# Kernel tuning notes

Measured on AMD Instinct MI355X. Metric: run time of the kernel, lower is better.

The kernel has to match this reference:

```python
import jax, jax.numpy as jnp
import numpy as np

B, N, E, C = 8, 4096, 1024, 512


def setup_inputs() -> dict:
    key = jax.random.key(0)
    k1, k2, k3, k4 = jax.random.split(key, 4)
    node_feats = jax.random.normal(k1, (B, N, C), dtype=jnp.float32)
    hyper_feats = jax.random.normal(k2, (B, E, C), dtype=jnp.float32)
    # torch nn.Linear params: weight [out, in], bias [out]
    Wq = jax.random.normal(k3, (C, C), dtype=jnp.float32) * (1.0 / np.sqrt(C))
    bq = jnp.zeros((C,), dtype=jnp.float32)
    Wkv = jax.random.normal(k4, (2 * C, C), dtype=jnp.float32) * (1.0 / np.sqrt(C))
    bkv = jnp.zeros((2 * C,), dtype=jnp.float32)
    return {"node_feats": node_feats, "hyper_feats": hyper_feats,
            "Wq": Wq, "bq": bq, "Wkv": Wkv, "bkv": bkv}


def reference(node_feats, hyper_feats, Wq, bq, Wkv, bkv):
    C_ = node_feats.shape[-1]
    scale = C_ ** -0.5
    Q = node_feats @ Wq.T + bq                      # [B,N,C]
    KV = hyper_feats @ Wkv.T + bkv                  # [B,E,2C]
    K, V = KV[..., :C_], KV[..., C_:]               # [B,E,C] each
    attn = jnp.einsum('bnc,bec->bne', Q, K) * scale  # [B,N,E]
    attn = jax.nn.softmax(attn, axis=-1)
    return jnp.einsum('bne,bec->bnc', attn, V)       # [B,N,C]
```

## Files before the change

### kernel.cpp

```cpp
#include <hip/hip_runtime.h>
#include <cstdint>
#include <cstddef>

typedef _Float16 h16;
typedef _Float16 h16x8 __attribute__((ext_vector_type(8)));
typedef float fx4 __attribute__((ext_vector_type(4)));

static constexpr int B_ = 8, N_ = 4096, E_ = 1024, C_ = 512;
static constexpr float SCALE = 0.044194173824159216f;

__device__ __forceinline__ void glds16(const h16* g, h16* l) {
  __builtin_amdgcn_global_load_lds(
      (const __attribute__((address_space(1))) unsigned int*)g,
      (__attribute__((address_space(3))) unsigned int*)l, 16, 0, 0);
}

__global__ __launch_bounds__(256) void cvt_kernel(const float* __restrict__ src,
                                                  h16* __restrict__ dst, int n8) {
  int i = blockIdx.x * 256 + threadIdx.x;
  if (i >= n8) return;
  const float4* s4 = (const float4*)src;
  float4 a = s4[2 * i], b = s4[2 * i + 1];
  h16x8 o;
  o[0] = (h16)a.x; o[1] = (h16)a.y; o[2] = (h16)a.z; o[3] = (h16)a.w;
  o[4] = (h16)b.x; o[5] = (h16)b.y; o[6] = (h16)b.z; o[7] = (h16)b.w;
  *(h16x8*)(dst + (size_t)i * 8) = o;
}

template <int MODE>
__global__ __launch_bounds__(256) void gemm_bt(
    const h16* __restrict__ A, const h16* __restrict__ Bm,
    const float* __restrict__ bias,
    h16* __restrict__ outH, h16* __restrict__ outK, h16* __restrict__ outV,
    float* __restrict__ outF,
    int Ncols, int K) {
  __shared__ h16 sA[128 * 32];
  __shared__ h16 sB[128 * 32];
  const int tid = threadIdx.x;
  const int wave = tid >> 6, lane = tid & 63;
  const int wm = wave >> 1, wn = wave & 1;
  const int lr = lane & 15, kq = lane >> 4;
  const int mBase = blockIdx.x * 128, nBase = blockIdx.y * 128;
  const int z = blockIdx.z;
  if (MODE == 2) { A += (size_t)z * N_ * C_; Bm += (size_t)z * E_ * C_; outH += (size_t)z * N_ * E_; }
  if (MODE == 3) { A += (size_t)z * N_ * E_; Bm += (size_t)z * C_ * E_; outF += (size_t)z * N_ * C_; }

  fx4 acc[4][4];
#pragma unroll
  for (int i = 0; i < 4; i++)
#pragma unroll
    for (int j = 0; j < 4; j++) acc[i][j] = (fx4){0.f, 0.f, 0.f, 0.f};

  const int rowInA = lane >> 2, colInA = (lane & 3) * 8;

  for (int kb = 0; kb < K; kb += 32) {
    __syncthreads();
#pragma unroll
    for (int i = 0; i < 2; i++) {
      int chunk = wave + i * 4;
      glds16(A + (size_t)(mBase + chunk * 16 + rowInA) * K + kb + colInA,
             &sA[chunk * 512]);
      glds16(Bm + (size_t)(nBase + chunk * 16 + rowInA) * K + kb + colInA,
             &sB[chunk * 512]);
    }
    __syncthreads();
    h16x8 af[4], bf[4];
#pragma unroll
    for (int mi = 0; mi < 4; mi++)
      af[mi] = *(const h16x8*)&sA[(wm * 64 + mi * 16 + lr) * 32 + kq * 8];
#pragma unroll
    for (int ni = 0; ni < 4; ni++)
      bf[ni] = *(const h16x8*)&sB[(wn * 64 + ni * 16 + lr) * 32 + kq * 8];
#pragma unroll
    for (int mi = 0; mi < 4; mi++)
#pragma unroll
      for (int ni = 0; ni < 4; ni++)
        acc[mi][ni] = __builtin_amdgcn_mfma_f32_16x16x32_f16(af[mi], bf[ni], acc[mi][ni], 0, 0, 0);
  }

  const int rb = kq * 4;
#pragma unroll
  for (int mi = 0; mi < 4; mi++) {
#pragma unroll
    for (int ni = 0; ni < 4; ni++) {
#pragma unroll
      for (int r = 0; r < 4; r++) {
        int row = mBase + wm * 64 + mi * 16 + rb + r;
        int col = nBase + wn * 64 + ni * 16 + lr;
        float v = acc[mi][ni][r];
        if (MODE == 0) {
          outH[(size_t)row * Ncols + col] = (h16)(v + bias[col]);
        } else if (MODE == 1) {
          v += bias[col];
          if (col < C_) outK[(size_t)row * C_ + col] = (h16)v;
          else          outV[(size_t)row * C_ + (col - C_)] = (h16)v;
        } else if (MODE == 2) {
          outH[(size_t)row * Ncols + col] = (h16)(v * SCALE);
        } else {
          outF[(size_t)row * Ncols + col] = v;
        }
      }
    }
  }
}

__global__ __launch_bounds__(256) void transpose_v(const h16* __restrict__ V,
                                                   h16* __restrict__ Vt) {
  __shared__ float t[64][65];
  int z = blockIdx.z;
  const h16* Vb = V + (size_t)z * E_ * C_;
  h16* Tb = Vt + (size_t)z * C_ * E_;
  int e0 = blockIdx.x * 64, c0 = blockIdx.y * 64;
  int tr = threadIdx.x >> 6, tc = threadIdx.x & 63;
#pragma unroll
  for (int p = 0; p < 16; p++)
    t[p * 4 + tr][tc] = (float)Vb[(size_t)(e0 + p * 4 + tr) * C_ + c0 + tc];
  __syncthreads();
#pragma unroll
  for (int p = 0; p < 16; p++)
    Tb[(size_t)(c0 + p * 4 + tr) * E_ + e0 + tc] = (h16)t[tc][p * 4 + tr];
}

__global__ __launch_bounds__(256) void softmax_rows(h16* __restrict__ S) {
  int row = blockIdx.x * 4 + (threadIdx.x >> 6);
  int lane = threadIdx.x & 63;
  h16* p = S + (size_t)row * E_ + lane * 16;
  h16x8 q0 = *(const h16x8*)p;
  h16x8 q1 = *(const h16x8*)(p + 8);
  float v[16];
#pragma unroll
  for (int j = 0; j < 8; j++) { v[j] = (float)q0[j]; v[8 + j] = (float)q1[j]; }
  float m = v[0];
#pragma unroll
  for (int j = 1; j < 16; j++) m = fmaxf(m, v[j]);
#pragma unroll
  for (int off = 32; off > 0; off >>= 1) m = fmaxf(m, __shfl_xor(m, off));
  float s = 0.f;
#pragma unroll
  for (int j = 0; j < 16; j++) { v[j] = __expf(v[j] - m); s += v[j]; }
#pragma unroll
  for (int off = 32; off > 0; off >>= 1) s += __shfl_xor(s, off);
  float inv = 1.f / s;
  h16x8 o0, o1;
#pragma unroll
  for (int j = 0; j < 8; j++) { o0[j] = (h16)(v[j] * inv); o1[j] = (h16)(v[8 + j] * inv); }
  *(h16x8*)p = o0;
  *(h16x8*)(p + 8) = o1;
}

extern "C" void kernel_launch(void* const* d_in, const int* in_sizes, int n_in,
                              void* d_out, int out_size, void* d_ws, size_t ws_size,
                              hipStream_t stream) {
  const float* node  = (const float*)d_in[0];
  const float* hyper = (const float*)d_in[1];
  const float* Wq    = (const float*)d_in[2];
  const float* bq    = (const float*)d_in[3];
  const float* Wkv   = (const float*)d_in[4];
  const float* bkv   = (const float*)d_in[5];
  float* out = (float*)d_out;
  char* ws = (char*)d_ws;

  h16* node_h  = (h16*)(ws + 0);
  h16* hyper_h = (h16*)(ws + 33554432);
  h16* Wq_h    = (h16*)(ws + 41943040);
  h16* Wkv_h   = (h16*)(ws + 42467328);
  h16* V_h     = (h16*)(ws + 43515904);
  h16* S_h     = (h16*)(ws + 0);
  h16* Q_h     = (h16*)(ws + 67108864);
  h16* K_h     = (h16*)(ws + 100663296);
  h16* Vt_h    = (h16*)(ws + 109051904);
  if (ws_size < 117440512u) return;

  cvt_kernel<<<dim3((B_ * N_ * C_ / 8 + 255) / 256), 256, 0, stream>>>(node, node_h, B_ * N_ * C_ / 8);
  cvt_kernel<<<dim3((B_ * E_ * C_ / 8 + 255) / 256), 256, 0, stream>>>(hyper, hyper_h, B_ * E_ * C_ / 8);
  cvt_kernel<<<dim3((C_ * C_ / 8 + 255) / 256), 256, 0, stream>>>(Wq, Wq_h, C_ * C_ / 8);
  cvt_kernel<<<dim3((2 * C_ * C_ / 8 + 255) / 256), 256, 0, stream>>>(Wkv, Wkv_h, 2 * C_ * C_ / 8);

  gemm_bt<0><<<dim3(B_ * N_ / 128, C_ / 128), 256, 0, stream>>>(
      node_h, Wq_h, bq, Q_h, nullptr, nullptr, nullptr, C_, C_);
  gemm_bt<1><<<dim3(B_ * E_ / 128, 2 * C_ / 128), 256, 0, stream>>>(
      hyper_h, Wkv_h, bkv, nullptr, K_h, V_h, nullptr, 2 * C_, C_);
  transpose_v<<<dim3(E_ / 64, C_ / 64, B_), 256, 0, stream>>>(V_h, Vt_h);
  gemm_bt<2><<<dim3(N_ / 128, E_ / 128, B_), 256, 0, stream>>>(
      Q_h, K_h, nullptr, S_h, nullptr, nullptr, nullptr, E_, C_);
  softmax_rows<<<dim3(B_ * N_ / 4), 256, 0, stream>>>(S_h);
  gemm_bt<3><<<dim3(N_ / 128, C_ / 128, B_), 256, 0, stream>>>(
      S_h, Vt_h, nullptr, nullptr, nullptr, nullptr, out, C_, E_);
}
```

Baseline: 328.4 us.

## Fuse fp32-to-fp16 input conversion into projection GEMMs and write V transposed

The projection GEMMs now read fp32 activations directly and convert them to fp16 while staging tiles into LDS. This removes the separate conversion passes over node and hyper features. The KV GEMM epilogue also writes V straight into the transposed layout with packed 4-element stores, so the transpose kernel is no longer needed. In exchange, the A-operand load becomes a synchronous register load plus LDS store instead of a direct global-to-LDS load, which may reduce load/compute overlap.

```diff
diff --git a/kernel.cpp b/kernel.cpp
--- a/kernel.cpp
+++ b/kernel.cpp
@@ -3,6 +3,7 @@
 #include <cstddef>
 
 typedef _Float16 h16;
+typedef _Float16 h16x4 __attribute__((ext_vector_type(4)));
 typedef _Float16 h16x8 __attribute__((ext_vector_type(8)));
 typedef float fx4 __attribute__((ext_vector_type(4)));
 
@@ -29,11 +30,12 @@
 
 template <int MODE>
 __global__ __launch_bounds__(256) void gemm_bt(
-    const h16* __restrict__ A, const h16* __restrict__ Bm,
+    const void* __restrict__ Ap, const h16* __restrict__ Bm,
     const float* __restrict__ bias,
-    h16* __restrict__ outH, h16* __restrict__ outK, h16* __restrict__ outV,
+    h16* __restrict__ outH, h16* __restrict__ outK, h16* __restrict__ outVt,
     float* __restrict__ outF,
     int Ncols, int K) {
+  constexpr bool CVT = (MODE <= 1);
   __shared__ h16 sA[128 * 32];
   __shared__ h16 sB[128 * 32];
   const int tid = threadIdx.x;
@@ -42,8 +44,10 @@
   const int lr = lane & 15, kq = lane >> 4;
   const int mBase = blockIdx.x * 128, nBase = blockIdx.y * 128;
   const int z = blockIdx.z;
-  if (MODE == 2) { A += (size_t)z * N_ * C_; Bm += (size_t)z * E_ * C_; outH += (size_t)z * N_ * E_; }
-  if (MODE == 3) { A += (size_t)z * N_ * E_; Bm += (size_t)z * C_ * E_; outF += (size_t)z * N_ * C_; }
+  const h16* Ah = (const h16*)Ap;
+  const float* Af = (const float*)Ap;
+  if (MODE == 2) { Ah += (size_t)z * N_ * C_; Bm += (size_t)z * E_ * C_; outH += (size_t)z * N_ * E_; }
+  if (MODE == 3) { Ah += (size_t)z * N_ * E_; Bm += (size_t)z * C_ * E_; outF += (size_t)z * N_ * C_; }
 
   fx4 acc[4][4];
 #pragma unroll
@@ -52,14 +56,31 @@
     for (int j = 0; j < 4; j++) acc[i][j] = (fx4){0.f, 0.f, 0.f, 0.f};
 
   const int rowInA = lane >> 2, colInA = (lane & 3) * 8;
+  const int cvtRow = tid >> 1, cvtCol = (tid & 1) * 16;
 
   for (int kb = 0; kb < K; kb += 32) {
     __syncthreads();
+    if (CVT) {
+      const float4* src = (const float4*)(Af + (size_t)(mBase + cvtRow) * K + kb + cvtCol);
+      float4 f0 = src[0], f1 = src[1], f2 = src[2], f3 = src[3];
+      h16x8 p0, p1;
+      p0[0] = (h16)f0.x; p0[1] = (h16)f0.y; p0[2] = (h16)f0.z; p0[3] = (h16)f0.w;
+      p0[4] = (h16)f1.x; p0[5] = (h16)f1.y; p0[6] = (h16)f1.z; p0[7] = (h16)f1.w;
+      p1[0] = (h16)f2.x; p1[1] = (h16)f2.y; p1[2] = (h16)f2.z; p1[3] = (h16)f2.w;
+      p1[4] = (h16)f3.x; p1[5] = (h16)f3.y; p1[6] = (h16)f3.z; p1[7] = (h16)f3.w;
+      *(h16x8*)&sA[cvtRow * 32 + cvtCol] = p0;
+      *(h16x8*)&sA[cvtRow * 32 + cvtCol + 8] = p1;
+    } else {
+#pragma unroll
+      for (int i = 0; i < 2; i++) {
+        int chunk = wave + i * 4;
+        glds16(Ah + (size_t)(mBase + chunk * 16 + rowInA) * K + kb + colInA,
+               &sA[chunk * 512]);
+      }
+    }
 #pragma unroll
     for (int i = 0; i < 2; i++) {
       int chunk = wave + i * 4;
-      glds16(A + (size_t)(mBase + chunk * 16 + rowInA) * K + kb + colInA,
-             &sA[chunk * 512]);
       glds16(Bm + (size_t)(nBase + chunk * 16 + rowInA) * K + kb + colInA,
              &sB[chunk * 512]);
     }
@@ -83,42 +104,33 @@
   for (int mi = 0; mi < 4; mi++) {
 #pragma unroll
     for (int ni = 0; ni < 4; ni++) {
+      int row0 = mBase + wm * 64 + mi * 16 + rb;
+      int col = nBase + wn * 64 + ni * 16 + lr;
+      if (MODE == 1 && col >= C_) {
+        float bv = bias[col];
+        h16x4 pk;
 #pragma unroll
-      for (int r = 0; r < 4; r++) {
-        int row = mBase + wm * 64 + mi * 16 + rb + r;
-        int col = nBase + wn * 64 + ni * 16 + lr;
-        float v = acc[mi][ni][r];
-        if (MODE == 0) {
-          outH[(size_t)row * Ncols + col] = (h16)(v + bias[col]);
-        } else if (MODE == 1) {
-          v += bias[col];
-          if (col < C_) outK[(size_t)row * C_ + col] = (h16)v;
-          else          outV[(size_t)row * C_ + (col - C_)] = (h16)v;
-        } else if (MODE == 2) {
-          outH[(size_t)row * Ncols + col] = (h16)(v * SCALE);
-        } else {
-          outF[(size_t)row * Ncols + col] = v;
+        for (int r = 0; r < 4; r++) pk[r] = (h16)(acc[mi][ni][r] + bv);
+        int zb = row0 >> 10, e = row0 & 1023;
+        *(h16x4*)&outVt[((size_t)zb * C_ + (col - C_)) * E_ + e] = pk;
+      } else {
+#pragma unroll
+        for (int r = 0; r < 4; r++) {
+          int row = row0 + r;
+          float v = acc[mi][ni][r];
+          if (MODE == 0) {
+            outH[(size_t)row * Ncols + col] = (h16)(v + bias[col]);
+          } else if (MODE == 1) {
+            outK[(size_t)row * C_ + col] = (h16)(v + bias[col]);
+          } else if (MODE == 2) {
+            outH[(size_t)row * Ncols + col] = (h16)(v * SCALE);
+          } else {
+            outF[(size_t)row * Ncols + col] = v;
+          }
         }
       }
     }
   }
-}
-
-__global__ __launch_bounds__(256) void transpose_v(const h16* __restrict__ V,
-                                                   h16* __restrict__ Vt) {
-  __shared__ float t[64][65];
-  int z = blockIdx.z;
-  const h16* Vb = V + (size_t)z * E_ * C_;
-  h16* Tb = Vt + (size_t)z * C_ * E_;
-  int e0 = blockIdx.x * 64, c0 = blockIdx.y * 64;
-  int tr = threadIdx.x >> 6, tc = threadIdx.x & 63;
-#pragma unroll
-  for (int p = 0; p < 16; p++)
-    t[p * 4 + tr][tc] = (float)Vb[(size_t)(e0 + p * 4 + tr) * C_ + c0 + tc];
-  __syncthreads();
-#pragma unroll
-  for (int p = 0; p < 16; p++)
-    Tb[(size_t)(c0 + p * 4 + tr) * E_ + e0 + tc] = (h16)t[tc][p * 4 + tr];
 }
 
 __global__ __launch_bounds__(256) void softmax_rows(h16* __restrict__ S) {
@@ -160,27 +172,21 @@
   float* out = (float*)d_out;
   char* ws = (char*)d_ws;
 
-  h16* node_h  = (h16*)(ws + 0);
-  h16* hyper_h = (h16*)(ws + 33554432);
-  h16* Wq_h    = (h16*)(ws + 41943040);
-  h16* Wkv_h   = (h16*)(ws + 42467328);
-  h16* V_h     = (h16*)(ws + 43515904);
-  h16* S_h     = (h16*)(ws + 0);
-  h16* Q_h     = (h16*)(ws + 67108864);
-  h16* K_h     = (h16*)(ws + 100663296);
-  h16* Vt_h    = (h16*)(ws + 109051904);
-  if (ws_size < 117440512u) return;
+  h16* S_h    = (h16*)(ws + 0);
+  h16* Q_h    = (h16*)(ws + 67108864);
+  h16* K_h    = (h16*)(ws + 100663296);
+  h16* Vt_h   = (h16*)(ws + 109051904);
+  h16* Wq_h   = (h16*)(ws + 117440512);
+  h16* Wkv_h  = (h16*)(ws + 117964800);
+  if (ws_size < 119013376u) return;
 
-  cvt_kernel<<<dim3((B_ * N_ * C_ / 8 + 255) / 256), 256, 0, stream>>>(node, node_h, B_ * N_ * C_ / 8);
-  cvt_kernel<<<dim3((B_ * E_ * C_ / 8 + 255) / 256), 256, 0, stream>>>(hyper, hyper_h, B_ * E_ * C_ / 8);
   cvt_kernel<<<dim3((C_ * C_ / 8 + 255) / 256), 256, 0, stream>>>(Wq, Wq_h, C_ * C_ / 8);
   cvt_kernel<<<dim3((2 * C_ * C_ / 8 + 255) / 256), 256, 0, stream>>>(Wkv, Wkv_h, 2 * C_ * C_ / 8);
 
   gemm_bt<0><<<dim3(B_ * N_ / 128, C_ / 128), 256, 0, stream>>>(
-      node_h, Wq_h, bq, Q_h, nullptr, nullptr, nullptr, C_, C_);
+      node, Wq_h, bq, Q_h, nullptr, nullptr, nullptr, C_, C_);
   gemm_bt<1><<<dim3(B_ * E_ / 128, 2 * C_ / 128), 256, 0, stream>>>(
-      hyper_h, Wkv_h, bkv, nullptr, K_h, V_h, nullptr, 2 * C_, C_);
-  transpose_v<<<dim3(E_ / 64, C_ / 64, B_), 256, 0, stream>>>(V_h, Vt_h);
+      hyper, Wkv_h, bkv, nullptr, K_h, Vt_h, nullptr, 2 * C_, C_);
   gemm_bt<2><<<dim3(N_ / 128, E_ / 128, B_), 256, 0, stream>>>(
       Q_h, K_h, nullptr, S_h, nullptr, nullptr, nullptr, E_, C_);
   softmax_rows<<<dim3(B_ * N_ / 4), 256, 0, stream>>>(S_h);
```

Result: faster. 314.2 us (-4.3%).
